# Kernel tuning notes

Measured on AMD Instinct MI355X. Metric: run time of the kernel, lower is better.

Reference implementation:

```python
import jax, jax.numpy as jnp
import numpy as np

# IO parameters (aihwkit-style preset)
INP_BOUND = 1.0
INP_RES = 1.0 / 254.0      # 8-bit DAC: 2^8 - 2 levels
OUT_BOUND = 12.0
OUT_RES = 1.0 / 510.0      # 9-bit ADC: 2^9 - 2 levels
OUT_NOISE = 0.06
OUT_SCALE = 1.0
MAX_BM_FACTOR = 1000.0
MAX_BM_RES = 0.25
INP_RES_EFF = 2.0 * INP_BOUND * INP_RES  # effective input grid step (bm escape test)


def _quantize_st(x, res, bound):
    # UniformQuantize: round to grid of step (res * 2 * bound), straight-through grad
    r = (1.0 / res if res > 1.0 else res) * 2.0 * bound
    q = jnp.round(x / r) * r
    return x + jax.lax.stop_gradient(q - x)


def _one_pass(input_, weight, nm, reduction, rnd, key):
    """One analog MVM pass at a given bound-management reduction factor."""
    scale = 1.0 / (nm * reduction)                      # [m, 1]
    x = input_ * scale                                  # noise/bound managed input
    x = _quantize_st(x, INP_RES, INP_BOUND)             # DAC discretization
    x = jnp.clip(x, -INP_BOUND, INP_BOUND)              # DAC clipping
    out = x @ weight.T                                  # [m, out_size] analog GEMM
    noise = OUT_NOISE * jax.random.normal(
        jax.random.fold_in(key, rnd), out.shape, out.dtype)
    out = out + noise                                   # output (ADC) noise
    out = _quantize_st(out, OUT_RES, OUT_BOUND)         # ADC discretization
    not_clipping = jnp.all((out <= OUT_BOUND) & (out >= -OUT_BOUND))
    out = jnp.clip(out, -OUT_BOUND, OUT_BOUND)          # ADC saturation
    return not_clipping, out


def setup_inputs() -> dict:
    key = jax.random.key(0)
    k1, k2 = jax.random.split(key)
    input_ = jax.random.normal(k1, (8192, 4096), jnp.float32)
    # 0.1 std weights -> outputs mostly within ADC bound after 1-2 bm rounds
    weight = 0.1 * jax.random.normal(k2, (4096, 4096), jnp.float32)
    return {"input_": input_, "weight": weight}


def reference(input_, weight):
    key = jax.random.key(42)
    # noise management: ABS_MAX over the input dimension (nm_thres <= 0 -> no clamp)
    nm = jnp.max(jnp.abs(input_), axis=-1, keepdims=True)
    nm = jnp.where(nm <= 0.0, 1.0, nm)
    out_shape = input_.shape[:-1] + (weight.shape[0],)

    def cond(c):
        return ~c[2]

    def body(c):
        rnd, red, _, _ = c
        red = red * 2.0          # reduction_due_to_bound_management *= 2
        rnd = rnd + 1
        passed, out = _one_pass(input_, weight, nm, red, rnd, key)
        passed = passed | (red > MAX_BM_FACTOR) | (red > MAX_BM_RES / INP_RES_EFF)
        return (rnd, red, passed, out)

    init = (jnp.int32(0), jnp.float32(0.5), jnp.array(False),
            jnp.zeros(out_shape, input_.dtype))
    _, red, _, out = jax.lax.while_loop(cond, body, init)
    # undo the input scaling: output *= out_scale / scale = out_scale * nm * red
    return out * (OUT_SCALE * nm * red)
```

## Files before the change

kernel.cpp:

```cpp
#include <hip/hip_runtime.h>
#include <stdint.h>


#define MM 8192
#define KK 4096
#define NN 4096
#define TOTAL_OUT ((size_t)MM * (size_t)NN)
#define GEMM_BLOCKS 2048
#define NT (KK / 64)

typedef __attribute__((ext_vector_type(4))) float f32x4;
typedef __attribute__((ext_vector_type(8))) short bf16x8;
typedef __attribute__((ext_vector_type(8))) unsigned short u16x8;

#define R_IN_F ((float)(2.0 / 254.0))
#define R_OUT_F ((float)(24.0 / 510.0))

struct BmState {
  int done;
  float red_final;
  int viol[8];
  int ctr[8];
};

__host__ __device__ __forceinline__ uint32_t tf_rotl(uint32_t v, int r) {
  return (v << r) | (v >> (32 - r));
}

__host__ __device__ __forceinline__ void threefry2x32(uint32_t k0, uint32_t k1,
                                                      uint32_t x0, uint32_t x1,
                                                      uint32_t &o0, uint32_t &o1) {
  uint32_t ks2 = k0 ^ k1 ^ 0x1BD11BDAu;
  x0 += k0; x1 += k1;
#define TF_R(r) { x0 += x1; x1 = tf_rotl(x1, r); x1 ^= x0; }
  TF_R(13) TF_R(15) TF_R(26) TF_R(6)
  x0 += k1; x1 += ks2 + 1u;
  TF_R(17) TF_R(29) TF_R(16) TF_R(24)
  x0 += ks2; x1 += k0 + 2u;
  TF_R(13) TF_R(15) TF_R(26) TF_R(6)
  x0 += k0; x1 += k1 + 3u;
  TF_R(17) TF_R(29) TF_R(16) TF_R(24)
  x0 += k1; x1 += ks2 + 4u;
  TF_R(13) TF_R(15) TF_R(26) TF_R(6)
  x0 += ks2; x1 += k0 + 5u;
#undef TF_R
  o0 = x0; o1 = x1;
}

__device__ __forceinline__ float erfinv_xla(float x) {
  float w = -log1pf(-x * x);
  float p;
  if (w < 5.0f) {
    w = w - 2.5f;
    p = 2.81022636e-08f;
    p = fmaf(p, w, 3.43273939e-07f);
    p = fmaf(p, w, -3.5233877e-06f);
    p = fmaf(p, w, -4.39150654e-06f);
    p = fmaf(p, w, 0.00021858087f);
    p = fmaf(p, w, -0.00125372503f);
    p = fmaf(p, w, -0.00417768164f);
    p = fmaf(p, w, 0.246640727f);
    p = fmaf(p, w, 1.50140941f);
  } else {
    w = sqrtf(w) - 3.0f;
    p = -0.000200214257f;
    p = fmaf(p, w, 0.000100950558f);
    p = fmaf(p, w, 0.00134934322f);
    p = fmaf(p, w, -0.00367342844f);
    p = fmaf(p, w, 0.00573950773f);
    p = fmaf(p, w, -0.0076224613f);
    p = fmaf(p, w, 0.00943887047f);
    p = fmaf(p, w, 1.00167406f);
    p = fmaf(p, w, 2.83297682f);
  }
  return p * x;
}

__device__ __forceinline__ float noise_from_bits(uint32_t bits) {
  uint32_t fb = (bits >> 9) | 0x3f800000u;
  float f = __uint_as_float(fb) - 1.0f;
  const float lo = -0.99999994f;
  float u = f * 2.0f + lo;
  u = fmaxf(lo, u);
  return 0.06f * (1.41421356f * erfinv_xla(u));
}

__device__ __forceinline__ unsigned short bf16_rne(float f) {
  uint32_t x = __float_as_uint(f);
  x += 0x7fffu + ((x >> 16) & 1u);
  return (unsigned short)(x >> 16);
}

__device__ __forceinline__ float dac_quant(float v, float s) {
  float x = v * s;
  float t = x / R_IN_F;
  float k = rintf(t);
  return fminf(127.0f, fmaxf(-127.0f, k));
}

__device__ __forceinline__ u16x8 quant8(float4 a, float4 b, float s) {
  u16x8 o;
  o[0] = bf16_rne(dac_quant(a.x, s));
  o[1] = bf16_rne(dac_quant(a.y, s));
  o[2] = bf16_rne(dac_quant(a.z, s));
  o[3] = bf16_rne(dac_quant(a.w, s));
  o[4] = bf16_rne(dac_quant(b.x, s));
  o[5] = bf16_rne(dac_quant(b.y, s));
  o[6] = bf16_rne(dac_quant(b.z, s));
  o[7] = bf16_rne(dac_quant(b.w, s));
  return o;
}

__device__ __forceinline__ u16x8 conv8(float4 a, float4 b) {
  u16x8 o;
  o[0] = bf16_rne(a.x); o[1] = bf16_rne(a.y); o[2] = bf16_rne(a.z); o[3] = bf16_rne(a.w);
  o[4] = bf16_rne(b.x); o[5] = bf16_rne(b.y); o[6] = bf16_rne(b.z); o[7] = bf16_rne(b.w);
  return o;
}

__device__ __forceinline__ float adc_one(float gval, size_t idx, float sc,
                                         uint32_t fk0, uint32_t fk1, bool &bad) {
  uint32_t w0, w1;
  threefry2x32(fk0, fk1, 0u, (uint32_t)idx, w0, w1);
  float o = R_IN_F * gval + noise_from_bits(w0 ^ w1);
  float q = rintf(o / R_OUT_F) * R_OUT_F;
  float z = o + (q - o);
  bad = bad || (z > 12.0f) || (z < -12.0f);
  z = fminf(12.0f, fmaxf(-12.0f, z));
  return z * sc;
}

__device__ __forceinline__ void fin_tail(BmState *st, int pass, float red, int nblocks,
                                         bool bad) {
  unsigned long long vb = __ballot(bad ? 1 : 0);
  if (vb != 0ull && (threadIdx.x & 63) == 0) atomicOr(&st->viol[pass], 1);
  __syncthreads();
  if (threadIdx.x == 0) {
    __threadfence();
    int prev = atomicAdd(&st->ctr[pass], 1);
    if (prev == nblocks - 1) {
      int viol = atomicOr(&st->viol[pass], 0);
      bool ok = (viol == 0) || (red > 1000.0f) || (red > 31.75f);
      if (ok) {
        st->done = 1;
        st->red_final = red;
      }
    }
  }
}

__global__ __launch_bounds__(256) void k_prep(const float *__restrict__ in,
                                              const float *__restrict__ w,
                                              float *__restrict__ nm,
                                              unsigned short *__restrict__ ab,
                                              unsigned short *__restrict__ wb,
                                              BmState *st) {
  const int t = threadIdx.x;
  if (blockIdx.x < MM) {
    if (blockIdx.x == 0 && t == 0) {
      st->done = 0;
      st->red_final = 0.0f;
      for (int i = 0; i < 8; ++i) { st->viol[i] = 0; st->ctr[i] = 0; }
    }
    const int row = blockIdx.x;
    const float *r = in + (size_t)row * KK;
    float4 a0 = *(const float4 *)(r + t * 8);
    float4 a1 = *(const float4 *)(r + t * 8 + 4);
    float4 b0 = *(const float4 *)(r + 2048 + t * 8);
    float4 b1 = *(const float4 *)(r + 2048 + t * 8 + 4);
    float m = 0.0f;
    m = fmaxf(m, fmaxf(fmaxf(fabsf(a0.x), fabsf(a0.y)), fmaxf(fabsf(a0.z), fabsf(a0.w))));
    m = fmaxf(m, fmaxf(fmaxf(fabsf(a1.x), fabsf(a1.y)), fmaxf(fabsf(a1.z), fabsf(a1.w))));
    m = fmaxf(m, fmaxf(fmaxf(fabsf(b0.x), fabsf(b0.y)), fmaxf(fabsf(b0.z), fabsf(b0.w))));
    m = fmaxf(m, fmaxf(fmaxf(fabsf(b1.x), fabsf(b1.y)), fmaxf(fabsf(b1.z), fabsf(b1.w))));
#pragma unroll
    for (int off = 32; off > 0; off >>= 1) m = fmaxf(m, __shfl_down(m, off));
    __shared__ float wm[4];
    if ((t & 63) == 0) wm[t >> 6] = m;
    __syncthreads();
    const float mm = fmaxf(fmaxf(wm[0], wm[1]), fmaxf(wm[2], wm[3]));
    const float nmv = (mm <= 0.0f) ? 1.0f : mm;
    if (t == 0) nm[row] = nmv;
    const float s = 1.0f / (nmv * 1.0f);
    unsigned short *o = ab + (size_t)row * KK;
    *(u16x8 *)(o + t * 8) = quant8(a0, a1, s);
    *(u16x8 *)(o + 2048 + t * 8) = quant8(b0, b1, s);
  } else {
    const size_t idx = ((size_t)(blockIdx.x - MM) * 256 + t) * 8;
    float4 a = *(const float4 *)(w + idx);
    float4 b = *(const float4 *)(w + idx + 4);
    *(u16x8 *)(wb + idx) = conv8(a, b);
  }
}

__global__ __launch_bounds__(256) void k_rowmax(const float *__restrict__ in,
                                                float *__restrict__ nm, BmState *st) {
  if (blockIdx.x == 0 && threadIdx.x == 0) {
    st->done = 0;
    st->red_final = 0.0f;
    for (int i = 0; i < 8; ++i) { st->viol[i] = 0; st->ctr[i] = 0; }
  }
  const int row = blockIdx.x;
  const float4 *r = (const float4 *)(in + (size_t)row * KK);
  const int t = threadIdx.x;
  float m = 0.0f;
#pragma unroll
  for (int i = 0; i < 4; ++i) {
    float4 v = r[t + i * 256];
    m = fmaxf(m, fmaxf(fmaxf(fabsf(v.x), fabsf(v.y)), fmaxf(fabsf(v.z), fabsf(v.w))));
  }
#pragma unroll
  for (int off = 32; off > 0; off >>= 1) m = fmaxf(m, __shfl_down(m, off));
  __shared__ float wm[4];
  if ((t & 63) == 0) wm[t >> 6] = m;
  __syncthreads();
  if (t == 0) {
    m = fmaxf(fmaxf(wm[0], wm[1]), fmaxf(wm[2], wm[3]));
    nm[row] = (m <= 0.0f) ? 1.0f : m;
  }
}

__device__ __forceinline__ void async16(const void *g, void *l) {
  __builtin_amdgcn_global_load_lds((const __attribute__((address_space(1))) uint32_t *)g,
                                   (__attribute__((address_space(3))) uint32_t *)l,
                                   16, 0, 0);
}

__global__ __launch_bounds__(512, 1) void k_gemm(const unsigned short *__restrict__ A,
                                                 const unsigned short *__restrict__ B,
                                                 float *__restrict__ C) {
  __shared__ unsigned short As[2][256 * 64];
  __shared__ unsigned short Bs[2][256 * 64];
  const int tid = threadIdx.x;
  const int lane = tid & 63;
  const int wv = tid >> 6;
  const int wr = wv >> 2;
  const int wc = wv & 3;
  const int brow = blockIdx.y * 256;
  const int bcol = blockIdx.x * 256;

  f32x4 acc[8][4];
#pragma unroll
  for (int m = 0; m < 8; ++m)
#pragma unroll
    for (int n = 0; n < 4; ++n) acc[m][n] = (f32x4){0.f, 0.f, 0.f, 0.f};

  int sr[4], sk8[4];
#pragma unroll
  for (int i = 0; i < 4; ++i) {
    const int u = i * 512 + tid;
    sr[i] = u >> 3;
    sk8[i] = ((u & 7) ^ (sr[i] & 7)) * 8;
  }

#define STAGE(buf, kt)                                                                 \
  {                                                                                    \
    _Pragma("unroll") for (int i = 0; i < 4; ++i) {                                    \
      const int ub = i * 512 + wv * 64;                \
      async16(A + (size_t)(brow + sr[i]) * KK + (kt) * 64 + sk8[i],                    \
              (char *)As[buf] + (size_t)ub * 16);                                      \
      async16(B + (size_t)(bcol + sr[i]) * KK + (kt) * 64 + sk8[i],                    \
              (char *)Bs[buf] + (size_t)ub * 16);                                      \
    }                                                                                  \
  }

  STAGE(0, 0);

  const int r16 = lane & 15;
  const int kg = (lane >> 4) * 8;

#pragma unroll 2
  for (int kt = 0; kt < NT; ++kt) {
    const int cur = kt & 1;
    if (kt + 1 < NT) {
      STAGE(cur ^ 1, kt + 1);
      asm volatile("s_waitcnt vmcnt(8)" ::: "memory");
    } else {
      asm volatile("s_waitcnt vmcnt(0)" ::: "memory");
    }
    __builtin_amdgcn_s_barrier();

#pragma unroll
    for (int kk = 0; kk < 64; kk += 32) {
      const int ck = (kk + kg) >> 3;
      bf16x8 af[8], bg[4];
#pragma unroll
      for (int m = 0; m < 8; ++m) {
        const int ra = wr * 128 + m * 16 + r16;
        af[m] = *(const bf16x8 *)(As[cur] + ra * 64 + ((ck ^ (ra & 7)) << 3));
      }
#pragma unroll
      for (int n = 0; n < 4; ++n) {
        const int rb = wc * 64 + n * 16 + r16;
        bg[n] = *(const bf16x8 *)(Bs[cur] + rb * 64 + ((ck ^ (rb & 7)) << 3));
      }
#pragma unroll
      for (int m = 0; m < 8; ++m)
#pragma unroll
        for (int n = 0; n < 4; ++n)
          acc[m][n] = __builtin_amdgcn_mfma_f32_16x16x32_bf16(af[m], bg[n], acc[m][n], 0, 0, 0);
    }
    __builtin_amdgcn_sched_barrier(0);
    __builtin_amdgcn_s_barrier();
  }
#undef STAGE

  const int c16 = lane & 15;
  const int q4 = (lane >> 4) * 4;
#pragma unroll
  for (int m = 0; m < 8; ++m) {
    const int row = brow + wr * 128 + m * 16 + q4;
#pragma unroll
    for (int n = 0; n < 4; ++n) {
      const int col = bcol + wc * 64 + n * 16 + c16;
      float *cp = C + (size_t)row * NN + col;
      cp[0 * (size_t)NN] = acc[m][n][0];
      cp[1 * (size_t)NN] = acc[m][n][1];
      cp[2 * (size_t)NN] = acc[m][n][2];
      cp[3 * (size_t)NN] = acc[m][n][3];
    }
  }
}

__global__ __launch_bounds__(256) void k_epi(float *__restrict__ out,
                                             const float *__restrict__ nm,
                                             BmState *__restrict__ st, int pass, float red,
                                             uint32_t fk0, uint32_t fk1) {
  const size_t idx = ((size_t)blockIdx.x * 256 + threadIdx.x) * 8;
  const int row = (int)(idx >> 12);
  const float sc = nm[row] * red;
  float4 a = *(const float4 *)(out + idx);
  float4 b = *(const float4 *)(out + idx + 4);
  float v[8] = {a.x, a.y, a.z, a.w, b.x, b.y, b.z, b.w};
  bool bad = false;
#pragma unroll
  for (int j = 0; j < 8; ++j) v[j] = adc_one(v[j], idx + j, sc, fk0, fk1, bad);
  *(float4 *)(out + idx) = make_float4(v[0], v[1], v[2], v[3]);
  *(float4 *)(out + idx + 4) = make_float4(v[4], v[5], v[6], v[7]);
  unsigned long long vb = __ballot(bad ? 1 : 0);
  if (vb != 0ull && (threadIdx.x & 63) == 0) atomicOr(&st->viol[pass], 1);
}

__global__ void k_fin(BmState *st, int pass, float red) {
  if (st->done) return;
  bool ok = (st->viol[pass] == 0) || (red > 1000.0f) || (red > 31.75f);
  if (ok) {
    st->done = 1;
    st->red_final = red;
  }
}

__global__ __launch_bounds__(256) void k_retry(const float *__restrict__ Af,
                                               const float *__restrict__ Bf,
                                               const float *__restrict__ nm, float red,
                                               float *__restrict__ C,
                                               BmState *__restrict__ st, int pass,
                                               uint32_t fk0, uint32_t fk1) {
  if (st->done) return;
  __shared__ unsigned short As[128 * 64];
  __shared__ unsigned short Bs[128 * 64];
  const int tid = threadIdx.x;
  const int lane = tid & 63;
  const int wv = tid >> 6;
  const int wr = wv >> 1, wc = wv & 1;
  const int brow = blockIdx.y * 128;
  const int bcol = blockIdx.x * 128;

  f32x4 acc[4][4];
#pragma unroll
  for (int m = 0; m < 4; ++m)
#pragma unroll
    for (int n = 0; n < 4; ++n) acc[m][n] = (f32x4){0.f, 0.f, 0.f, 0.f};

  float sA[4];
#pragma unroll
  for (int i = 0; i < 4; ++i) {
    int u = i * 256 + tid;
    sA[i] = 1.0f / (nm[brow + (u >> 3)] * red);
  }

  for (int kt = 0; kt < KK; kt += 64) {
#pragma unroll
    for (int i = 0; i < 4; ++i) {
      const int u = i * 256 + tid;
      const int r = u >> 3, k8 = (u & 7) * 8;
      {
        const float *g = Af + (size_t)(brow + r) * KK + kt + k8;
        float4 x = *(const float4 *)g, y = *(const float4 *)(g + 4);
        *(u16x8 *)(As + r * 64 + k8) = quant8(x, y, sA[i]);
      }
      {
        const float *g = Bf + (size_t)(bcol + r) * KK + kt + k8;
        float4 x = *(const float4 *)g, y = *(const float4 *)(g + 4);
        *(u16x8 *)(Bs + r * 64 + k8) = conv8(x, y);
      }
    }
    __syncthreads();

    const int r16 = lane & 15;
    const int kg = (lane >> 4) * 8;
#pragma unroll
    for (int kk = 0; kk < 64; kk += 32) {
      bf16x8 af[4], bg[4];
#pragma unroll
      for (int m = 0; m < 4; ++m)
        af[m] = *(const bf16x8 *)(As + (wr * 64 + m * 16 + r16) * 64 + kk + kg);
#pragma unroll
      for (int n = 0; n < 4; ++n)
        bg[n] = *(const bf16x8 *)(Bs + (wc * 64 + n * 16 + r16) * 64 + kk + kg);
#pragma unroll
      for (int m = 0; m < 4; ++m)
#pragma unroll
        for (int n = 0; n < 4; ++n)
          acc[m][n] = __builtin_amdgcn_mfma_f32_16x16x32_bf16(af[m], bg[n], acc[m][n], 0, 0, 0);
    }
    __syncthreads();
  }

  const int c16 = lane & 15;
  const int q4 = (lane >> 4) * 4;
  bool bad = false;
#pragma unroll
  for (int m = 0; m < 4; ++m) {
    const int row0 = brow + wr * 64 + m * 16 + q4;
#pragma unroll
    for (int j = 0; j < 4; ++j) {
      const int row = row0 + j;
      const float sc = nm[row] * red;
#pragma unroll
      for (int n = 0; n < 4; ++n) {
        const int col = bcol + wc * 64 + n * 16 + c16;
        const size_t idx = (size_t)row * NN + col;
        C[idx] = adc_one(acc[m][n][j], idx, sc, fk0, fk1, bad);
      }
    }
  }
  fin_tail(st, pass, red, GEMM_BLOCKS, bad);
}

extern "C" void kernel_launch(void *const *d_in, const int *in_sizes, int n_in,
                              void *d_out, int out_size, void *d_ws, size_t ws_size,
                              hipStream_t stream) {
  const float *input = (const float *)d_in[0];
  const float *weight = (const float *)d_in[1];
  if (n_in >= 2 && in_sizes[0] < in_sizes[1]) {
    const float *t = input; input = weight; weight = t;
  }
  float *out = (float *)d_out;
  char *ws = (char *)d_ws;
  BmState *st = (BmState *)ws;
  float *nm = (float *)(ws + 4096);
  unsigned short *Ab = (unsigned short *)(ws + 36864);
  unsigned short *Wb = Ab + (size_t)MM * KK;
  const size_t need = 36864 + ((size_t)MM * KK + (size_t)NN * KK) * 2;
  const bool fast = ws_size >= need;

  uint32_t fk[8][2];
  for (int p = 1; p <= 6; ++p) threefry2x32(0u, 42u, 0u, (uint32_t)p, fk[p][0], fk[p][1]);

  if (fast) {
    k_prep<<<dim3(MM + (NN * (size_t)KK) / 2048), dim3(256), 0, stream>>>(
        input, weight, nm, Ab, Wb, st);
    k_gemm<<<dim3(NN / 256, MM / 256), dim3(512), 0, stream>>>(Ab, Wb, out);
    k_epi<<<dim3((int)(TOTAL_OUT / 2048)), dim3(256), 0, stream>>>(out, nm, st, 1, 1.0f,
                                                                   fk[1][0], fk[1][1]);
    k_fin<<<dim3(1), dim3(1), 0, stream>>>(st, 1, 1.0f);
  } else {
    k_rowmax<<<dim3(MM), dim3(256), 0, stream>>>(input, nm, st);
    k_retry<<<dim3(NN / 128, MM / 128), dim3(256), 0, stream>>>(
        input, weight, nm, 1.0f, out, st, 1, fk[1][0], fk[1][1]);
  }

  float red = 2.0f;
  for (int p = 2; p <= 6; ++p, red *= 2.0f) {
    k_retry<<<dim3(NN / 128, MM / 128), dim3(256), 0, stream>>>(
        input, weight, nm, red, out, st, p, fk[p][0], fk[p][1]);
  }
}
```

Before: 490.6 us.

## Split GEMM k-tile into four phases interleaving LDS reads with prioritized MFMA clusters

Restructures the inner k-tile loop of the bf16 GEMM into four phases. B fragments for the whole tile are loaded once up front, then each phase loads A fragments for two m-rows and runs their MFMAs. Barriers around each MFMA cluster plus s_setprio(1) are meant to stagger waves so that one wave's LDS reads overlap another's matrix math, in a ping-pong style schedule. The cost is more barriers per tile and more live B registers, so the gain depends on whether waves actually interleave.

Measured after the change: 518.3 us. +5.6%, slower.

```diff
diff --git a/kernel.cpp b/kernel.cpp
--- a/kernel.cpp
+++ b/kernel.cpp
@@ -267,7 +267,7 @@
   STAGE(0, 0);
 
   const int r16 = lane & 15;
-  const int kg = (lane >> 4) * 8;
+  const int kgc = lane >> 4;
 
 #pragma unroll 2
   for (int kt = 0; kt < NT; ++kt) {
@@ -280,28 +280,44 @@
     }
     __builtin_amdgcn_s_barrier();
 
-#pragma unroll
-    for (int kk = 0; kk < 64; kk += 32) {
-      const int ck = (kk + kg) >> 3;
-      bf16x8 af[8], bg[4];
-#pragma unroll
-      for (int m = 0; m < 8; ++m) {
-        const int ra = wr * 128 + m * 16 + r16;
-        af[m] = *(const bf16x8 *)(As[cur] + ra * 64 + ((ck ^ (ra & 7)) << 3));
+    bf16x8 bg[2][4];
+#pragma unroll
+    for (int q = 0; q < 4; ++q) {
+      if (q == 0) {
+#pragma unroll
+        for (int x = 0; x < 2; ++x)
+#pragma unroll
+          for (int n = 0; n < 4; ++n) {
+            const int rb = wc * 64 + n * 16 + r16;
+            bg[x][n] = *(const bf16x8 *)(Bs[cur] + rb * 64 +
+                                         (((x * 4 + kgc) ^ (rb & 7)) << 3));
+          }
       }
-#pragma unroll
-      for (int n = 0; n < 4; ++n) {
-        const int rb = wc * 64 + n * 16 + r16;
-        bg[n] = *(const bf16x8 *)(Bs[cur] + rb * 64 + ((ck ^ (rb & 7)) << 3));
-      }
-#pragma unroll
-      for (int m = 0; m < 8; ++m)
-#pragma unroll
-        for (int n = 0; n < 4; ++n)
-          acc[m][n] = __builtin_amdgcn_mfma_f32_16x16x32_bf16(af[m], bg[n], acc[m][n], 0, 0, 0);
-    }
-    __builtin_amdgcn_sched_barrier(0);
-    __builtin_amdgcn_s_barrier();
+      bf16x8 af[2][2];
+#pragma unroll
+      for (int x = 0; x < 2; ++x)
+#pragma unroll
+        for (int mm = 0; mm < 2; ++mm) {
+          const int ra = wr * 128 + (2 * q + mm) * 16 + r16;
+          af[x][mm] = *(const bf16x8 *)(As[cur] + ra * 64 +
+                                        (((x * 4 + kgc) ^ (ra & 7)) << 3));
+        }
+      if (q == 0) asm volatile("s_waitcnt lgkmcnt(8)" ::: "memory");
+      __builtin_amdgcn_s_barrier();
+      asm volatile("s_waitcnt lgkmcnt(0)" ::: "memory");
+      __builtin_amdgcn_sched_barrier(0);
+      __builtin_amdgcn_s_setprio(1);
+#pragma unroll
+      for (int x = 0; x < 2; ++x)
+#pragma unroll
+        for (int mm = 0; mm < 2; ++mm)
+#pragma unroll
+          for (int n = 0; n < 4; ++n)
+            acc[2 * q + mm][n] = __builtin_amdgcn_mfma_f32_16x16x32_bf16(
+                af[x][mm], bg[x][n], acc[2 * q + mm][n], 0, 0, 0);
+      __builtin_amdgcn_s_setprio(0);
+      __builtin_amdgcn_s_barrier();
+    }
   }
 #undef STAGE
 
```
